# Kernel tuning notes

Measured on AMD Instinct MI355X. Metric: run time of the kernel, lower is better.

Reference implementation:

```python
import jax, jax.numpy as jnp
import numpy as np

N = 20000        # nodes
E = 320000       # directed edges (before self-loops)
HEADS = 4
IN_DIM = 256
HID = [256, 128]
ZD = [128, 64]
S = 10           # num_samples in reparameterize
REAL_MIN = 2.2e-10
THETA_MAX = 1000.0
KMIN, KMAX = 0.1, 1000.0
SLOPE = 0.2      # GATConv leaky_relu negative_slope


def setup_inputs() -> dict:
    key = jax.random.key(0)
    ks = jax.random.split(key, 24)
    f32 = jnp.float32
    def p(k, shape, scale):
        return jax.random.normal(k, shape, dtype=f32) * scale
    inp = {}
    inp["x"] = jax.random.normal(ks[0], (N, IN_DIM), dtype=f32)
    inp["edge_index"] = jax.random.randint(ks[1], (2, E), 0, N)
    # layer 0: GAT 256 -> 4 heads x 64 (concat = 256)
    inp["gatW0"] = p(ks[2], (HID[0], IN_DIM), 0.06)
    inp["asrc0"] = p(ks[3], (HEADS, HID[0] // HEADS), 0.1)
    inp["adst0"] = p(ks[4], (HEADS, HID[0] // HEADS), 0.1)
    inp["gatb0"] = p(ks[5], (HID[0],), 0.02)
    inp["fcW0"] = p(ks[6], (ZD[0], HID[0]), 0.06)
    inp["fcb0"] = p(ks[7], (ZD[0],), 0.02)
    inp["shW0"] = p(ks[8], (ZD[0], ZD[0]), 0.08)
    inp["shb0"] = p(ks[9], (ZD[0],), 0.02)
    inp["scW0"] = p(ks[10], (ZD[0], ZD[0]), 0.08)
    inp["scb0"] = p(ks[11], (ZD[0],), 0.02)
    # layer 1: GAT 256 -> 4 heads x 32 (concat = 128)
    inp["gatW1"] = p(ks[12], (HID[1], HID[0]), 0.06)
    inp["asrc1"] = p(ks[13], (HEADS, HID[1] // HEADS), 0.1)
    inp["adst1"] = p(ks[14], (HEADS, HID[1] // HEADS), 0.1)
    inp["gatb1"] = p(ks[15], (HID[1],), 0.02)
    inp["fcW1"] = p(ks[16], (ZD[1], HID[1]), 0.06)
    inp["fcb1"] = p(ks[17], (ZD[1],), 0.02)
    inp["shW1"] = p(ks[18], (ZD[1], ZD[1]), 0.08)
    inp["shb1"] = p(ks[19], (ZD[1],), 0.02)
    inp["scW1"] = p(ks[20], (ZD[1], ZD[1]), 0.08)
    inp["scb1"] = p(ks[21], (ZD[1],), 0.02)
    # Weibull reparameterization noise eps ~ U(0,1), shape (S, z_dim, N)
    inp["eps0"] = jax.random.uniform(ks[22], (S, ZD[0], N), dtype=f32)
    inp["eps1"] = jax.random.uniform(ks[23], (S, ZD[1], N), dtype=f32)
    return inp


def _gat(x, src, dst, W, a_src, a_dst, b):
    """PyG GATConv (shared lin, concat heads, add_self_loops done by caller)."""
    n = x.shape[0]
    xw = (x @ W.T).reshape(n, HEADS, -1)            # [N, H, C]
    s = (xw * a_src[None]).sum(-1)                  # [N, H] alpha_src
    d = (xw * a_dst[None]).sum(-1)                  # [N, H] alpha_dst
    e = s[src] + d[dst]                             # [E, H]
    e = jnp.where(e > 0, e, SLOPE * e)              # leaky_relu
    m = jax.lax.stop_gradient(jax.ops.segment_max(e, dst, num_segments=n))
    ex = jnp.exp(e - m[dst])
    den = jax.ops.segment_sum(ex, dst, num_segments=n)
    alpha = ex / (den[dst] + 1e-16)                 # segment softmax over in-edges
    out = jax.ops.segment_sum(alpha[:, :, None] * xw[src], dst, num_segments=n)
    return out.reshape(n, -1) + b                   # [N, H*C]


def _reparam(k, l, eps):
    # theta = l * (-log(max(1-eps, real_min)))^(1/k), mean over samples, clamp
    lm = jnp.log(jnp.maximum(1.0 - eps, REAL_MIN))  # [S, z, N]
    theta = l[None] * jnp.power(-lm, 1.0 / k[None])
    return jnp.clip(theta.mean(0), REAL_MIN, THETA_MAX)


def _right(h, Wk, bk, Wl, bl, eps):
    k = jnp.clip(jax.nn.softplus(h @ Wk.T + bk).T, KMIN, KMAX)      # [z, N]
    l = jnp.maximum(jax.nn.softplus(h @ Wl.T + bl).T, REAL_MIN)     # [z, N]
    l = l / jnp.exp(jax.lax.lgamma(1.0 + 1.0 / k))
    return _reparam(k, l, eps), k, l


def reference(x, edge_index, gatW0, asrc0, adst0, gatb0, fcW0, fcb0, shW0, shb0,
              scW0, scb0, gatW1, asrc1, adst1, gatb1, fcW1, fcb1, shW1, shb1,
              scW1, scb1, eps0, eps1):
    n = x.shape[0]
    loops = jnp.arange(n)
    src = jnp.concatenate([edge_index[0], loops])   # GATConv add_self_loops
    dst = jnp.concatenate([edge_index[1], loops])
    h0 = _gat(x, src, dst, gatW0, asrc0, adst0, gatb0)
    z0 = jax.nn.softplus(h0 @ fcW0.T + fcb0)
    h1 = _gat(h0, src, dst, gatW1, asrc1, adst1, gatb1)
    z1 = jax.nn.softplus(h1 @ fcW1.T + fcb1)
    theta1, k1, l1 = _right(z1, shW1, shb1, scW1, scb1, eps1)
    theta0, k0, l0 = _right(z0, shW0, shb0, scW0, scb0, eps0)
    return (theta0, theta1, k0, k1, l0, l1)
```

## Files before the change

### kernel.cpp

```cpp
#include <hip/hip_runtime.h>
#include <math.h>

#define N_NODES 20000
#define E_EDGES 320000
#define NHEADS 4
#define RMIN 2.2e-10f
#define THETA_MAX 1000.0f
#define SLOPE 0.2f
#define LOG2E 1.4426950408889634f
#define LOG2_LN2 -0.5287663729448977f

__device__ __forceinline__ float softplus_f(float x) {
    return fmaxf(x, 0.0f) + log1pf(expf(-fabsf(x)));
}

__device__ __forceinline__ float ew1(float sv, float dh) {
    float e = (sv + dh) * LOG2E;
    e = e > 0.f ? e : SLOPE * e;
    return __builtin_amdgcn_exp2f(e);
}

__global__ __launch_bounds__(256) void count_kernel(const int* __restrict__ dst,
                                                    int* __restrict__ deg) {
    int e = blockIdx.x * 256 + threadIdx.x;
    if (e < E_EDGES) atomicAdd(&deg[dst[e]], 1);
}

__global__ __launch_bounds__(256) void scan_kernel(const int* __restrict__ deg,
                                                   int* __restrict__ rowptr,
                                                   int* __restrict__ cursor) {
    __shared__ int part[256];
    int t = threadIdx.x;
    const int CH = (N_NODES + 255) / 256;
    int base = t * CH;
    int sum = 0;
    for (int i = 0; i < CH; ++i) {
        int idx = base + i;
        if (idx < N_NODES) sum += deg[idx];
    }
    part[t] = sum;
    __syncthreads();
    for (int off = 1; off < 256; off <<= 1) {
        int v = (t >= off) ? part[t - off] : 0;
        __syncthreads();
        part[t] += v;
        __syncthreads();
    }
    int run = (t == 0) ? 0 : part[t - 1];
    for (int i = 0; i < CH; ++i) {
        int idx = base + i;
        if (idx < N_NODES) {
            rowptr[idx] = run;
            cursor[idx] = run;
            run += deg[idx];
        }
    }
    if (t == 255) rowptr[N_NODES] = run;
}

__global__ __launch_bounds__(256) void scatter_kernel(const int* __restrict__ src,
                                                      const int* __restrict__ dst,
                                                      int* __restrict__ cursor,
                                                      int* __restrict__ csr) {
    int e = blockIdx.x * 256 + threadIdx.x;
    if (e < E_EDGES) {
        int p = atomicAdd(&cursor[dst[e]], 1);
        csr[p] = src[e];
    }
}

template <int MODE, bool TRANS>
__device__ __forceinline__ void gemm_epilogue4(const float acc[4][4],
                                               const float* __restrict__ bp,
                                               float* __restrict__ op,
                                               int ow, int colbase, int r0, int lc, int M) {
    float bv[4] = {0.f, 0.f, 0.f, 0.f};
    if (MODE != 0) *(float4*)bv = *(const float4*)(bp + colbase + lc);
    float vals[4][4];
#pragma unroll
    for (int i = 0; i < 4; ++i)
#pragma unroll
        for (int j = 0; j < 4; ++j) {
            float v = acc[i][j];
            if (MODE == 1) v = softplus_f(v + bv[j]);
            else if (MODE == 2) { v = softplus_f(v + bv[j]); v = fminf(fmaxf(v, 0.1f), 1000.0f); }
            else if (MODE == 3) { v = fmaxf(softplus_f(v + bv[j]), RMIN); }
            vals[i][j] = v;
        }
    if (!TRANS) {
#pragma unroll
        for (int i = 0; i < 4; ++i) {
            int row = r0 + i;
            if (row < M) *(float4*)(op + (size_t)row * ow + colbase + lc) = *(float4*)vals[i];
        }
    } else {
        if (r0 + 3 < M) {
#pragma unroll
            for (int j = 0; j < 4; ++j) {
                int c = colbase + lc + j;
                float col[4] = {vals[0][j], vals[1][j], vals[2][j], vals[3][j]};
                *(float4*)(op + (size_t)c * M + r0) = *(float4*)col;
            }
        } else {
#pragma unroll
            for (int i = 0; i < 4; ++i) {
                int row = r0 + i;
                if (row < M)
#pragma unroll
                    for (int j = 0; j < 4; ++j) op[(size_t)(colbase + lc + j) * M + row] = vals[i][j];
            }
        }
    }
}

template <int MODE0, int MODE1, bool TRANS, int SDW, int CPER>
__global__ __launch_bounds__(256) void gemm64_kernel(const float* __restrict__ A,
                                                     const float* __restrict__ W0,
                                                     const float* __restrict__ W1,
                                                     const float* __restrict__ b0p,
                                                     const float* __restrict__ b1p,
                                                     float* __restrict__ out0,
                                                     float* __restrict__ out1,
                                                     const float* __restrict__ asrc,
                                                     const float* __restrict__ adst,
                                                     float* __restrict__ sp,
                                                     float* __restrict__ dp,
                                                     int M, int K, int split, int no1) {
    __shared__ float As[16][68];
    __shared__ float Bs[16][68];
    int tid = threadIdx.x;
    int tx = tid & 15, ty = tid >> 4;
    int bm = blockIdx.x * 64;
    int bn = blockIdx.y * 64;
    bool first = bn < split;
    const float* W = first ? (W0 + (size_t)bn * K) : (W1 + (size_t)(bn - split) * K);
    int m = tid >> 2;
    int kk0 = (tid & 3) * 4;
    int arow = bm + m;
    bool avalid = arow < M;
    const float* Ap = A + (size_t)arow * K + kk0;
    const float* Wp = W + (size_t)m * K + kk0;

    float4 av = make_float4(0.f, 0.f, 0.f, 0.f);
    if (avalid) av = *(const float4*)(Ap);
    float4 bv = *(const float4*)(Wp);

    float acc[4][4] = {};
    int T = K >> 4;
    for (int t = 0; t < T; ++t) {
        As[kk0 + 0][m] = av.x; As[kk0 + 1][m] = av.y;
        As[kk0 + 2][m] = av.z; As[kk0 + 3][m] = av.w;
        Bs[kk0 + 0][m] = bv.x; Bs[kk0 + 1][m] = bv.y;
        Bs[kk0 + 2][m] = bv.z; Bs[kk0 + 3][m] = bv.w;
        __syncthreads();
        if (t + 1 < T) {
            int ko = (t + 1) << 4;
            if (avalid) av = *(const float4*)(Ap + ko);
            bv = *(const float4*)(Wp + ko);
        }
#pragma unroll
        for (int kk = 0; kk < 16; ++kk) {
            float a[4], b[4];
            *(float4*)a = *(const float4*)(&As[kk][ty * 4]);
            *(float4*)b = *(const float4*)(&Bs[kk][tx * 4]);
#pragma unroll
            for (int i = 0; i < 4; ++i)
#pragma unroll
                for (int j = 0; j < 4; ++j) acc[i][j] += a[i] * b[j];
        }
        __syncthreads();
    }
    int r0 = bm + ty * 4;
    int lc = tx * 4;

    if constexpr (SDW != 0) {
        bool dosd = (SDW == 1) ? first : !first;
        if (dosd) {
            int bo = (SDW == 1) ? bn : bn - split;
            float4 as4 = *(const float4*)(asrc + bo + lc);
            float4 ad4 = *(const float4*)(adst + bo + lc);
            float ps[4], pd[4];
#pragma unroll
            for (int i = 0; i < 4; ++i) {
                ps[i] = acc[i][0] * as4.x + acc[i][1] * as4.y + acc[i][2] * as4.z + acc[i][3] * as4.w;
                pd[i] = acc[i][0] * ad4.x + acc[i][1] * ad4.y + acc[i][2] * ad4.z + acc[i][3] * ad4.w;
            }
#pragma unroll
            for (int off = (CPER == 64 ? 8 : 4); off >= 1; off >>= 1) {
#pragma unroll
                for (int i = 0; i < 4; ++i) {
                    ps[i] += __shfl_xor(ps[i], off, 64);
                    pd[i] += __shfl_xor(pd[i], off, 64);
                }
            }
            bool lanesel;
            int h;
            if constexpr (CPER == 64) { lanesel = (tx == 0); h = bo >> 6; }
            else { lanesel = ((tx & 7) == 0); h = (bo >> 5) + (tx >> 3); }
            if (lanesel) {
#pragma unroll
                for (int i = 0; i < 4; ++i) {
                    int row = r0 + i;
                    if (row < M) {
                        sp[row * NHEADS + h] = ps[i];
                        dp[row * NHEADS + h] = pd[i];
                    }
                }
            }
        }
    }

    if (first) gemm_epilogue4<MODE0, TRANS>(acc, b0p, out0, split, bn, r0, lc, M);
    else       gemm_epilogue4<MODE1, TRANS>(acc, b1p, out1, no1, bn - split, r0, lc, M);
}

__global__ __launch_bounds__(256) void gemmC_kernel(const float* __restrict__ h1,
                                                    const float* __restrict__ fcW1,
                                                    const float* __restrict__ fcb1,
                                                    float* __restrict__ z1,
                                                    const float* __restrict__ z0,
                                                    const float* __restrict__ shW0,
                                                    const float* __restrict__ shb0,
                                                    float* __restrict__ k0,
                                                    const float* __restrict__ scW0,
                                                    const float* __restrict__ scb0,
                                                    float* __restrict__ l0,
                                                    int M) {
    constexpr int K = 128;
    __shared__ float As[16][68];
    __shared__ float Bs[16][68];
    int tid = threadIdx.x;
    int tx = tid & 15, ty = tid >> 4;
    int bm = blockIdx.x * 64;
    int y = blockIdx.y;
    const float* A;
    const float* W;
    if (y == 0)      { A = h1; W = fcW1; }
    else if (y <= 2) { A = z0; W = shW0 + (size_t)(y - 1) * 64 * K; }
    else             { A = z0; W = scW0 + (size_t)(y - 3) * 64 * K; }
    int m = tid >> 2;
    int kk0 = (tid & 3) * 4;
    int arow = bm + m;
    bool avalid = arow < M;
    const float* Ap = A + (size_t)arow * K + kk0;
    const float* Wp = W + (size_t)m * K + kk0;

    float4 av = make_float4(0.f, 0.f, 0.f, 0.f);
    if (avalid) av = *(const float4*)(Ap);
    float4 bv = *(const float4*)(Wp);

    float acc[4][4] = {};
    constexpr int T = K >> 4;
    for (int t = 0; t < T; ++t) {
        As[kk0 + 0][m] = av.x; As[kk0 + 1][m] = av.y;
        As[kk0 + 2][m] = av.z; As[kk0 + 3][m] = av.w;
        Bs[kk0 + 0][m] = bv.x; Bs[kk0 + 1][m] = bv.y;
        Bs[kk0 + 2][m] = bv.z; Bs[kk0 + 3][m] = bv.w;
        __syncthreads();
        if (t + 1 < T) {
            int ko = (t + 1) << 4;
            if (avalid) av = *(const float4*)(Ap + ko);
            bv = *(const float4*)(Wp + ko);
        }
#pragma unroll
        for (int kk = 0; kk < 16; ++kk) {
            float a[4], b[4];
            *(float4*)a = *(const float4*)(&As[kk][ty * 4]);
            *(float4*)b = *(const float4*)(&Bs[kk][tx * 4]);
#pragma unroll
            for (int i = 0; i < 4; ++i)
#pragma unroll
                for (int j = 0; j < 4; ++j) acc[i][j] += a[i] * b[j];
        }
        __syncthreads();
    }
    int r0 = bm + ty * 4;
    int lc = tx * 4;
    if (y == 0)      gemm_epilogue4<1, false>(acc, fcb1, z1, 64, 0, r0, lc, M);
    else if (y <= 2) gemm_epilogue4<2, true>(acc, shb0, k0, 128, (y - 1) * 64, r0, lc, M);
    else             gemm_epilogue4<3, true>(acc, scb0, l0, 128, (y - 3) * 64, r0, lc, M);
}

template <int F>
__global__ __launch_bounds__(256) void agg_kernel(const float* __restrict__ xw,
                                                  const int* __restrict__ rowptr,
                                                  const int* __restrict__ csr,
                                                  const float* __restrict__ s,
                                                  const float* __restrict__ d,
                                                  const float* __restrict__ bias,
                                                  float* __restrict__ out) {
    constexpr int VEC = F / 64;
    int wave = threadIdx.x >> 6;
    int lane = threadIdx.x & 63;
    int n = blockIdx.x * 4 + wave;
    if (n >= N_NODES) return;
    int c0 = lane * VEC;
    int h = lane >> 4;

    float dh = d[(size_t)n * NHEADS + h];
    float w = ew1(s[(size_t)n * NHEADS + h], dh);
    float den = w;
    float acc[VEC];
    {
        float r[VEC];
        const float* rp = xw + (size_t)n * F + c0;
        if constexpr (VEC == 4) *(float4*)r = *(const float4*)rp;
        else                    *(float2*)r = *(const float2*)rp;
#pragma unroll
        for (int v = 0; v < VEC; ++v) acc[v] = w * r[v];
    }

    int idx = rowptr[n], end = rowptr[n + 1];
    for (; idx + 4 <= end; idx += 4) {
        int n0 = csr[idx], n1 = csr[idx + 1], n2 = csr[idx + 2], n3 = csr[idx + 3];
        float w0 = ew1(s[(size_t)n0 * NHEADS + h], dh);
        float w1 = ew1(s[(size_t)n1 * NHEADS + h], dh);
        float w2 = ew1(s[(size_t)n2 * NHEADS + h], dh);
        float w3 = ew1(s[(size_t)n3 * NHEADS + h], dh);
        den += w0; den += w1; den += w2; den += w3;
        float r0[VEC], r1[VEC], r2[VEC], r3[VEC];
        const float* p0 = xw + (size_t)n0 * F + c0;
        const float* p1 = xw + (size_t)n1 * F + c0;
        const float* p2 = xw + (size_t)n2 * F + c0;
        const float* p3 = xw + (size_t)n3 * F + c0;
        if constexpr (VEC == 4) {
            *(float4*)r0 = *(const float4*)p0; *(float4*)r1 = *(const float4*)p1;
            *(float4*)r2 = *(const float4*)p2; *(float4*)r3 = *(const float4*)p3;
        } else {
            *(float2*)r0 = *(const float2*)p0; *(float2*)r1 = *(const float2*)p1;
            *(float2*)r2 = *(const float2*)p2; *(float2*)r3 = *(const float2*)p3;
        }
#pragma unroll
        for (int v = 0; v < VEC; ++v) {
            acc[v] += w0 * r0[v];
            acc[v] += w1 * r1[v];
            acc[v] += w2 * r2[v];
            acc[v] += w3 * r3[v];
        }
    }
    for (; idx < end; ++idx) {
        int n0 = csr[idx];
        float w0 = ew1(s[(size_t)n0 * NHEADS + h], dh);
        den += w0;
        float r0[VEC];
        const float* p0 = xw + (size_t)n0 * F + c0;
        if constexpr (VEC == 4) *(float4*)r0 = *(const float4*)p0;
        else                    *(float2*)r0 = *(const float2*)p0;
#pragma unroll
        for (int v = 0; v < VEC; ++v) acc[v] += w0 * r0[v];
    }

    float rden = 1.0f / (den + 1e-16f);
    float o[VEC], bvv[VEC];
    const float* bp = bias + c0;
    if constexpr (VEC == 4) *(float4*)bvv = *(const float4*)bp;
    else                    *(float2*)bvv = *(const float2*)bp;
#pragma unroll
    for (int v = 0; v < VEC; ++v) o[v] = acc[v] * rden + bvv[v];
    float* op = out + (size_t)n * F + c0;
    if constexpr (VEC == 4) *(float4*)op = *(float4*)o;
    else                    *(float2*)op = *(float2*)o;
}

__device__ __forceinline__ void theta_work(const float* __restrict__ eps,
                                           const float* __restrict__ kptr,
                                           float* __restrict__ lptr,
                                           float* __restrict__ theta, int i, int ZN) {
    float k = kptr[i];
    float invk = __builtin_amdgcn_rcpf(k);
    float lg = lgammaf(1.0f + invk);
    float l = lptr[i] * __builtin_amdgcn_exp2f(-lg * LOG2E);
    lptr[i] = l;
    float c = invk * LOG2_LN2;
    float acc = 0.0f;
#pragma unroll
    for (int ss = 0; ss < 10; ++ss) {
        float u = eps[(size_t)ss * ZN + i];
        float t = -__builtin_amdgcn_logf(fmaxf(1.0f - u, RMIN));
        acc += __builtin_amdgcn_exp2f(invk * __builtin_amdgcn_logf(t) + c);
    }
    float th = l * acc * 0.1f;
    th = fminf(fmaxf(th, RMIN), THETA_MAX);
    theta[i] = th;
}

__global__ __launch_bounds__(256) void theta2_kernel(const float* __restrict__ eps0,
                                                     float* __restrict__ k0,
                                                     float* __restrict__ l0,
                                                     float* __restrict__ th0,
                                                     const float* __restrict__ eps1,
                                                     float* __restrict__ k1,
                                                     float* __restrict__ l1,
                                                     float* __restrict__ th1) {
    int i = blockIdx.x * 256 + threadIdx.x;
    if (i < 2560000) {
        theta_work(eps0, k0, l0, th0, i, 2560000);
    } else {
        int j = i - 2560000;
        if (j < 1280000) theta_work(eps1, k1, l1, th1, j, 1280000);
    }
}

extern "C" void kernel_launch(void* const* d_in, const int* in_sizes, int n_in,
                              void* d_out, int out_size, void* d_ws, size_t ws_size,
                              hipStream_t stream) {
    const float* x     = (const float*)d_in[0];
    const int*   eidx  = (const int*)d_in[1];
    const float* gatW0 = (const float*)d_in[2];
    const float* asrc0 = (const float*)d_in[3];
    const float* adst0 = (const float*)d_in[4];
    const float* gatb0 = (const float*)d_in[5];
    const float* fcW0  = (const float*)d_in[6];
    const float* fcb0  = (const float*)d_in[7];
    const float* shW0  = (const float*)d_in[8];
    const float* shb0  = (const float*)d_in[9];
    const float* scW0  = (const float*)d_in[10];
    const float* scb0  = (const float*)d_in[11];
    const float* gatW1 = (const float*)d_in[12];
    const float* asrc1 = (const float*)d_in[13];
    const float* adst1 = (const float*)d_in[14];
    const float* gatb1 = (const float*)d_in[15];
    const float* fcW1  = (const float*)d_in[16];
    const float* fcb1  = (const float*)d_in[17];
    const float* shW1  = (const float*)d_in[18];
    const float* shb1  = (const float*)d_in[19];
    const float* scW1  = (const float*)d_in[20];
    const float* scb1  = (const float*)d_in[21];
    const float* eps0  = (const float*)d_in[22];
    const float* eps1  = (const float*)d_in[23];

    const int* e_src = eidx;
    const int* e_dst = eidx + E_EDGES;

    size_t off = 0;
    auto carve = [&](size_t elems) {
        void* p = (char*)d_ws + off;
        off += ((elems * 4 + 255) / 256) * 256;
        return p;
    };
    float* xw0 = (float*)carve(20000u * 256);
    float* h0  = (float*)carve(20000u * 256);
    float* z0  = (float*)carve(20000u * 128);
    float* xw1 = (float*)carve(20000u * 128);
    float* h1  = (float*)carve(20000u * 128);
    float* z1  = (float*)carve(20000u * 64);
    float* s0  = (float*)carve(20000u * 4);
    float* d0  = (float*)carve(20000u * 4);
    float* s1  = (float*)carve(20000u * 4);
    float* d1  = (float*)carve(20000u * 4);
    int* deg    = (int*)carve(20000);
    int* rowptr = (int*)carve(20001);
    int* cursor = (int*)carve(20000);
    int* csr    = (int*)carve(E_EDGES);

    float* out    = (float*)d_out;
    float* theta0 = out;
    float* theta1 = out + 2560000;
    float* k0     = out + 3840000;
    float* k1     = out + 6400000;
    float* l0     = out + 7680000;
    float* l1     = out + 10240000;

    const int M = N_NODES;
    dim3 blk(256);
    const int GX = (N_NODES + 63) / 64;

    (void)hipMemsetAsync(deg, 0, N_NODES * sizeof(int), stream);
    count_kernel<<<(E_EDGES + 255) / 256, blk, 0, stream>>>(e_dst, deg);
    scan_kernel<<<1, blk, 0, stream>>>(deg, rowptr, cursor);
    scatter_kernel<<<(E_EDGES + 255) / 256, blk, 0, stream>>>(e_src, e_dst, cursor, csr);

    gemm64_kernel<0, 0, false, 1, 64><<<dim3(GX, 4), blk, 0, stream>>>(
        x, gatW0, nullptr, nullptr, nullptr, xw0, nullptr,
        asrc0, adst0, s0, d0, M, 256, 256, 0);
    agg_kernel<256><<<5000, blk, 0, stream>>>(xw0, rowptr, csr, s0, d0, gatb0, h0);

    gemm64_kernel<1, 0, false, 2, 32><<<dim3(GX, 4), blk, 0, stream>>>(
        h0, fcW0, gatW1, fcb0, nullptr, z0, xw1,
        asrc1, adst1, s1, d1, M, 256, 128, 128);
    agg_kernel<128><<<5000, blk, 0, stream>>>(xw1, rowptr, csr, s1, d1, gatb1, h1);

    gemmC_kernel<<<dim3(GX, 5), blk, 0, stream>>>(
        h1, fcW1, fcb1, z1, z0, shW0, shb0, k0, scW0, scb0, l0, M);

    gemm64_kernel<2, 3, true, 0, 64><<<dim3(GX, 2), blk, 0, stream>>>(
        z1, shW1, scW1, shb1, scb1, k1, l1,
        nullptr, nullptr, nullptr, nullptr, M, 64, 64, 64);

    theta2_kernel<<<15000, blk, 0, stream>>>(eps0, k0, l0, theta0, eps1, k1, l1, theta1);
}
```

Measured before the change: 562.7 us.

## Use bf16x3-split MFMA GEMMs for GAT projections and move attention dots to separate kernel

Replaces the FP32 SIMT GEMMs for the two GAT projection layers with an MFMA kernel that splits each fp32 operand into three bf16 parts and accumulates six bf16 products, to emulate near-fp32 precision on matrix cores. The per-head attention source/destination dot products, previously fused into the GEMM epilogue, now run in a new sd_kernel that rereads xw from memory. This trades extra conversion work, LDS traffic and an extra kernel pass for higher matrix throughput.

```diff
diff --git a/kernel.cpp b/kernel.cpp
--- a/kernel.cpp
+++ b/kernel.cpp
@@ -10,6 +10,10 @@
 #define LOG2E 1.4426950408889634f
 #define LOG2_LN2 -0.5287663729448977f
 
+typedef unsigned short ushort_t;
+typedef __attribute__((ext_vector_type(8))) short bf16x8;
+typedef __attribute__((ext_vector_type(4))) float f32x4;
+
 __device__ __forceinline__ float softplus_f(float x) {
     return fmaxf(x, 0.0f) + log1pf(expf(-fabsf(x)));
 }
@@ -18,6 +22,16 @@
     float e = (sv + dh) * LOG2E;
     e = e > 0.f ? e : SLOPE * e;
     return __builtin_amdgcn_exp2f(e);
+}
+
+__device__ __forceinline__ void split3(float a, ushort_t &h, ushort_t &m, ushort_t &l) {
+    unsigned u = __float_as_uint(a);
+    h = (ushort_t)(u >> 16);
+    float r1 = a - __uint_as_float(u & 0xFFFF0000u);
+    unsigned v = __float_as_uint(r1);
+    m = (ushort_t)(v >> 16);
+    float r2 = r1 - __uint_as_float(v & 0xFFFF0000u);
+    l = (ushort_t)(__float_as_uint(r2) >> 16);
 }
 
 __global__ __launch_bounds__(256) void count_kernel(const int* __restrict__ dst,
@@ -69,6 +83,154 @@
     }
 }
 
+__device__ __forceinline__ void stage3(float4 f0, float4 f1, ushort_t (*lds)[64][40],
+                                       int row, int k8) {
+    float f[8] = {f0.x, f0.y, f0.z, f0.w, f1.x, f1.y, f1.z, f1.w};
+    bf16x8 v1, v2, v3;
+#pragma unroll
+    for (int j = 0; j < 8; ++j) {
+        ushort_t h, m, l;
+        split3(f[j], h, m, l);
+        v1[j] = (short)h; v2[j] = (short)m; v3[j] = (short)l;
+    }
+    *(bf16x8*)&lds[0][row][k8] = v1;
+    *(bf16x8*)&lds[1][row][k8] = v2;
+    *(bf16x8*)&lds[2][row][k8] = v3;
+}
+
+template <int MODE>
+__device__ __forceinline__ void epilogueM(const f32x4 acc[2][2], const float* __restrict__ bp,
+                                          float* __restrict__ op, int ow, int colbase,
+                                          int bm, int wr, int wc, int lane, int M) {
+#pragma unroll
+    for (int rt = 0; rt < 2; ++rt) {
+#pragma unroll
+        for (int ct = 0; ct < 2; ++ct) {
+            int col = colbase + wc * 32 + ct * 16 + (lane & 15);
+            float bv = (MODE != 0) ? bp[col] : 0.f;
+#pragma unroll
+            for (int r = 0; r < 4; ++r) {
+                int m = bm + wr * 32 + rt * 16 + (lane >> 4) * 4 + r;
+                if (m < M) {
+                    float v = acc[rt][ct][r];
+                    if (MODE == 1) v = softplus_f(v + bv);
+                    op[(size_t)m * ow + col] = v;
+                }
+            }
+        }
+    }
+}
+
+template <int MODE0, int MODE1>
+__global__ __launch_bounds__(256) void gemmM_kernel(const float* __restrict__ A,
+                                                    const float* __restrict__ W0,
+                                                    const float* __restrict__ W1,
+                                                    const float* __restrict__ b0p,
+                                                    const float* __restrict__ b1p,
+                                                    float* __restrict__ out0,
+                                                    float* __restrict__ out1,
+                                                    int M, int K, int split,
+                                                    int ow0, int ow1) {
+    __shared__ ushort_t Alds[3][64][40];
+    __shared__ ushort_t Blds[3][64][40];
+    int tid = threadIdx.x;
+    int lane = tid & 63, w = tid >> 6, wr = w >> 1, wc = w & 1;
+    int bm = blockIdx.x * 64, bn = blockIdx.y * 64;
+    bool first = bn < split;
+    const float* Wb = first ? (W0 + (size_t)bn * K) : (W1 + (size_t)(bn - split) * K);
+    int srow = tid >> 2;
+    int sk8 = (tid & 3) * 8;
+    int arow_g = bm + srow;
+    bool avalid = arow_g < M;
+    const float* Ap = A + (size_t)arow_g * K + sk8;
+    const float* Wp = Wb + (size_t)srow * K + sk8;
+
+    float4 a0 = make_float4(0.f, 0.f, 0.f, 0.f), a1 = a0;
+    if (avalid) { a0 = *(const float4*)(Ap); a1 = *(const float4*)(Ap + 4); }
+    float4 b0 = *(const float4*)(Wp), b1 = *(const float4*)(Wp + 4);
+
+    f32x4 acc[2][2];
+#pragma unroll
+    for (int i = 0; i < 2; ++i)
+#pragma unroll
+        for (int j = 0; j < 2; ++j) acc[i][j] = (f32x4){0.f, 0.f, 0.f, 0.f};
+
+    int T = K >> 5;
+    for (int t = 0; t < T; ++t) {
+        stage3(a0, a1, Alds, srow, sk8);
+        stage3(b0, b1, Blds, srow, sk8);
+        __syncthreads();
+        if (t + 1 < T) {
+            int ko = (t + 1) << 5;
+            if (avalid) { a0 = *(const float4*)(Ap + ko); a1 = *(const float4*)(Ap + ko + 4); }
+            b0 = *(const float4*)(Wp + ko); b1 = *(const float4*)(Wp + ko + 4);
+        }
+        int koff = (lane >> 4) * 8;
+#pragma unroll
+        for (int rt = 0; rt < 2; ++rt) {
+            int ar = wr * 32 + rt * 16 + (lane & 15);
+            bf16x8 A1 = *(const bf16x8*)&Alds[0][ar][koff];
+            bf16x8 A2 = *(const bf16x8*)&Alds[1][ar][koff];
+            bf16x8 A3 = *(const bf16x8*)&Alds[2][ar][koff];
+#pragma unroll
+            for (int ct = 0; ct < 2; ++ct) {
+                int br = wc * 32 + ct * 16 + (lane & 15);
+                bf16x8 B1 = *(const bf16x8*)&Blds[0][br][koff];
+                bf16x8 B2 = *(const bf16x8*)&Blds[1][br][koff];
+                bf16x8 B3 = *(const bf16x8*)&Blds[2][br][koff];
+                f32x4 c = acc[rt][ct];
+                c = __builtin_amdgcn_mfma_f32_16x16x32_bf16(A1, B3, c, 0, 0, 0);
+                c = __builtin_amdgcn_mfma_f32_16x16x32_bf16(A3, B1, c, 0, 0, 0);
+                c = __builtin_amdgcn_mfma_f32_16x16x32_bf16(A2, B2, c, 0, 0, 0);
+                c = __builtin_amdgcn_mfma_f32_16x16x32_bf16(A1, B2, c, 0, 0, 0);
+                c = __builtin_amdgcn_mfma_f32_16x16x32_bf16(A2, B1, c, 0, 0, 0);
+                c = __builtin_amdgcn_mfma_f32_16x16x32_bf16(A1, B1, c, 0, 0, 0);
+                acc[rt][ct] = c;
+            }
+        }
+        __syncthreads();
+    }
+    if (first) epilogueM<MODE0>(acc, b0p, out0, ow0, bn, bm, wr, wc, lane, M);
+    else       epilogueM<MODE1>(acc, b1p, out1, ow1, bn - split, bm, wr, wc, lane, M);
+}
+
+template <int F, int CPER>
+__global__ __launch_bounds__(256) void sd_kernel(const float* __restrict__ xw,
+                                                 const float* __restrict__ asrc,
+                                                 const float* __restrict__ adst,
+                                                 float* __restrict__ s,
+                                                 float* __restrict__ d) {
+    int wave = threadIdx.x >> 6;
+    int lane = threadIdx.x & 63;
+    int n = blockIdx.x * 4 + wave;
+    if (n >= N_NODES) return;
+    float ss[NHEADS] = {0, 0, 0, 0}, dd[NHEADS] = {0, 0, 0, 0};
+#pragma unroll
+    for (int j = 0; j < F / 64; ++j) {
+        int c = j * 64 + lane;
+        int h = c / CPER;
+        int cc = c % CPER;
+        float v = xw[(size_t)n * F + c];
+        ss[h] += v * asrc[h * CPER + cc];
+        dd[h] += v * adst[h * CPER + cc];
+    }
+#pragma unroll
+    for (int off = 32; off > 0; off >>= 1) {
+#pragma unroll
+        for (int h = 0; h < NHEADS; ++h) {
+            ss[h] += __shfl_xor(ss[h], off, 64);
+            dd[h] += __shfl_xor(dd[h], off, 64);
+        }
+    }
+    if (lane == 0) {
+#pragma unroll
+        for (int h = 0; h < NHEADS; ++h) {
+            s[n * NHEADS + h] = ss[h];
+            d[n * NHEADS + h] = dd[h];
+        }
+    }
+}
+
 template <int MODE, bool TRANS>
 __device__ __forceinline__ void gemm_epilogue4(const float acc[4][4],
                                                const float* __restrict__ bp,
@@ -113,7 +275,7 @@
     }
 }
 
-template <int MODE0, int MODE1, bool TRANS, int SDW, int CPER>
+template <int MODE0, int MODE1, bool TRANS>
 __global__ __launch_bounds__(256) void gemm64_kernel(const float* __restrict__ A,
                                                      const float* __restrict__ W0,
                                                      const float* __restrict__ W1,
@@ -121,10 +283,6 @@
                                                      const float* __restrict__ b1p,
                                                      float* __restrict__ out0,
                                                      float* __restrict__ out1,
-                                                     const float* __restrict__ asrc,
-                                                     const float* __restrict__ adst,
-                                                     float* __restrict__ sp,
-                                                     float* __restrict__ dp,
                                                      int M, int K, int split, int no1) {
     __shared__ float As[16][68];
     __shared__ float Bs[16][68];
@@ -172,44 +330,6 @@
     }
     int r0 = bm + ty * 4;
     int lc = tx * 4;
-
-    if constexpr (SDW != 0) {
-        bool dosd = (SDW == 1) ? first : !first;
-        if (dosd) {
-            int bo = (SDW == 1) ? bn : bn - split;
-            float4 as4 = *(const float4*)(asrc + bo + lc);
-            float4 ad4 = *(const float4*)(adst + bo + lc);
-            float ps[4], pd[4];
-#pragma unroll
-            for (int i = 0; i < 4; ++i) {
-                ps[i] = acc[i][0] * as4.x + acc[i][1] * as4.y + acc[i][2] * as4.z + acc[i][3] * as4.w;
-                pd[i] = acc[i][0] * ad4.x + acc[i][1] * ad4.y + acc[i][2] * ad4.z + acc[i][3] * ad4.w;
-            }
-#pragma unroll
-            for (int off = (CPER == 64 ? 8 : 4); off >= 1; off >>= 1) {
-#pragma unroll
-                for (int i = 0; i < 4; ++i) {
-                    ps[i] += __shfl_xor(ps[i], off, 64);
-                    pd[i] += __shfl_xor(pd[i], off, 64);
-                }
-            }
-            bool lanesel;
-            int h;
-            if constexpr (CPER == 64) { lanesel = (tx == 0); h = bo >> 6; }
-            else { lanesel = ((tx & 7) == 0); h = (bo >> 5) + (tx >> 3); }
-            if (lanesel) {
-#pragma unroll
-                for (int i = 0; i < 4; ++i) {
-                    int row = r0 + i;
-                    if (row < M) {
-                        sp[row * NHEADS + h] = ps[i];
-                        dp[row * NHEADS + h] = pd[i];
-                    }
-                }
-            }
-        }
-    }
-
     if (first) gemm_epilogue4<MODE0, TRANS>(acc, b0p, out0, split, bn, r0, lc, M);
     else       gemm_epilogue4<MODE1, TRANS>(acc, b1p, out1, no1, bn - split, r0, lc, M);
 }
@@ -470,22 +590,21 @@
     scan_kernel<<<1, blk, 0, stream>>>(deg, rowptr, cursor);
     scatter_kernel<<<(E_EDGES + 255) / 256, blk, 0, stream>>>(e_src, e_dst, cursor, csr);
 
-    gemm64_kernel<0, 0, false, 1, 64><<<dim3(GX, 4), blk, 0, stream>>>(
-        x, gatW0, nullptr, nullptr, nullptr, xw0, nullptr,
-        asrc0, adst0, s0, d0, M, 256, 256, 0);
+    gemmM_kernel<0, 0><<<dim3(GX, 4), blk, 0, stream>>>(
+        x, gatW0, nullptr, nullptr, nullptr, xw0, nullptr, M, 256, 256, 256, 0);
+    sd_kernel<256, 64><<<5000, blk, 0, stream>>>(xw0, asrc0, adst0, s0, d0);
     agg_kernel<256><<<5000, blk, 0, stream>>>(xw0, rowptr, csr, s0, d0, gatb0, h0);
 
-    gemm64_kernel<1, 0, false, 2, 32><<<dim3(GX, 4), blk, 0, stream>>>(
-        h0, fcW0, gatW1, fcb0, nullptr, z0, xw1,
-        asrc1, adst1, s1, d1, M, 256, 128, 128);
+    gemmM_kernel<1, 0><<<dim3(GX, 4), blk, 0, stream>>>(
+        h0, fcW0, gatW1, fcb0, nullptr, z0, xw1, M, 256, 128, 128, 128);
+    sd_kernel<128, 32><<<5000, blk, 0, stream>>>(xw1, asrc1, adst1, s1, d1);
     agg_kernel<128><<<5000, blk, 0, stream>>>(xw1, rowptr, csr, s1, d1, gatb1, h1);
 
     gemmC_kernel<<<dim3(GX, 5), blk, 0, stream>>>(
         h1, fcW1, fcb1, z1, z0, shW0, shb0, k0, scW0, scb0, l0, M);
 
-    gemm64_kernel<2, 3, true, 0, 64><<<dim3(GX, 2), blk, 0, stream>>>(
-        z1, shW1, scW1, shb1, scb1, k1, l1,
-        nullptr, nullptr, nullptr, nullptr, M, 64, 64, 64);
+    gemm64_kernel<2, 3, true><<<dim3(GX, 2), blk, 0, stream>>>(
+        z1, shW1, scW1, shb1, scb1, k1, l1, M, 64, 64, 64);
 
     theta2_kernel<<<15000, blk, 0, stream>>>(eps0, k0, l0, theta0, eps1, k1, l1, theta1);
 }
```

Result: no change. 563.4 us (+0.1%).
